# Kernel optimization log

Hardware: AMD Instinct MI355X
Metric: run time of the kernel (lower is better)

## Reference

```python
import jax, jax.numpy as jnp
import numpy as np

N = 4096
HID = 512
NUM_HEADS = 8
HEAD_DIM = HID // NUM_HEADS
SCALING = HID ** (-0.5)


def setup_inputs() -> dict:
    key = jax.random.key(0)
    k0, k1, k2, k3, k4, k5 = jax.random.split(key, 6)
    h = jax.random.normal(k0, (N, HID), dtype=jnp.float32)
    A = (jax.random.uniform(k1, (N, N), dtype=jnp.float32) < 0.01).astype(jnp.float32)
    scale = 0.02
    Wq = jax.random.normal(k2, (HID, HID), dtype=jnp.float32) * scale
    Wk = jax.random.normal(k3, (HID, HID), dtype=jnp.float32) * scale
    Wv = jax.random.normal(k4, (HID, HID), dtype=jnp.float32) * scale
    Wo = jax.random.normal(k5, (HID, HID), dtype=jnp.float32) * scale
    return {"A": A, "h": h, "Wq": Wq, "Wk": Wk, "Wv": Wv, "Wo": Wo}


def reference(A, h, Wq, Wk, Wv, Wo):
    n = h.shape[0]
    # nn.Linear: y = x @ W.T ; reshape(N, head_dim, num_heads) puts heads LAST
    q = (h @ Wq.T).reshape(n, HEAD_DIM, NUM_HEADS) * SCALING  # [N, D, H]
    k = (h @ Wk.T).reshape(n, HEAD_DIM, NUM_HEADS)            # [N, D, H]
    v = (h @ Wv.T).reshape(n, HEAD_DIM, NUM_HEADS)            # [N, D, H]
    # scores = bmm(q^T[H,N,D], k^T[H,D,N]) -> [H, N, N]
    scores = jnp.einsum('ndh,mdh->hnm', q, k)
    # mask by dense multiply (zeros still contribute exp(0) to softmax, as in source)
    attn = jax.nn.softmax(A[None, :, :] * scores, axis=-1)    # [H, N, N]
    # out = bmm(attn, v^T[H,N,D]) -> [H, N, D] -> transpose to [N, D, H]
    out = jnp.einsum('hnm,mdh->ndh', attn, v)                 # [N, D, H]
    out = out.reshape(n, HEAD_DIM * NUM_HEADS) @ Wo.T         # [N, HID]
    return out
```

## Files before the change

### kernel.cpp

```cpp
#include <hip/hip_runtime.h>
#include <hip/hip_bf16.h>


#define N_TOK 4096
#define HID   512
#define NHEAD 8
#define HDIM  64
#define SCALING_F 0.044194173824159216f

#define QH_OFF    0u
#define KVB_OFF   2097152u
#define VSP_OFF   3145728u
#define VSUM_OFF  3162112u
#define CNT_OFF   3162624u
#define LIST_OFF  3166720u
#define HB_OFF    3691008u
#define WQKV_OFF  4739584u
#define WO_OFF    5132800u

typedef __attribute__((ext_vector_type(8))) short bf16x8;
typedef __attribute__((ext_vector_type(4))) float f32x4;
typedef __attribute__((ext_vector_type(2))) float f32x2;

__device__ __forceinline__ ushort f2bf(float f) {
    union { float f; unsigned u; } x; x.f = f;
    const unsigned r = x.u + 0x7fffu + ((x.u >> 16) & 1u);
    return (ushort)(r >> 16);
}

#define GLOAD_LDS16(g, l) \
    __builtin_amdgcn_global_load_lds((const __attribute__((address_space(1))) void*)(g), \
                                     (__attribute__((address_space(3))) void*)(l), 16, 0, 0)

__global__ __launch_bounds__(256) void prep(const float* __restrict__ A,
                                            const float* __restrict__ h,
                                            const float* __restrict__ wq,
                                            const float* __restrict__ wk,
                                            const float* __restrict__ wv,
                                            const float* __restrict__ wo,
                                            float* __restrict__ ws)
{
    const int bx = blockIdx.x;
    if (bx < 1024) {
        int* cnts  = (int*)(ws + CNT_OFF);
        int* lists = (int*)(ws + LIST_OFF);
        const int row  = bx * 4 + (threadIdx.x >> 6);
        const int lane = threadIdx.x & 63;
        const float4* Arow = (const float4*)(A + (size_t)row * N_TOK);
        int* out = lists + (size_t)row * 128;
        int cnt = 0;
#pragma unroll 4
        for (int it = 0; it < 16; ++it) {
            const float4 v = Arow[it * 64 + lane];
            const float vals[4] = {v.x, v.y, v.z, v.w};
#pragma unroll
            for (int j = 0; j < 4; ++j) {
                const bool nz = (vals[j] != 0.0f);
                const unsigned long long mask = __ballot(nz);
                if (nz) {
                    const int pos = cnt + __popcll(mask & ((1ull << lane) - 1ull));
                    if (pos < 128) out[pos] = it * 256 + lane * 4 + j;
                }
                cnt += __popcll(mask);
            }
        }
        if (lane == 0) cnts[row] = (cnt < 128) ? cnt : 128;
        return;
    }

    const int cb    = bx - 1024;
    const int chunk = cb >> 8;
    const int inner = (cb & 255) * 1024 + threadIdx.x * 4;
    ushort* hb    = (ushort*)(ws + HB_OFF);
    ushort* wqkvb = (ushort*)(ws + WQKV_OFF);
    ushort* wob   = (ushort*)(ws + WO_OFF);

    if (chunk < 11) {
        const float* src;
        ushort* dst;
        if (chunk < 8)       { src = h + (size_t)chunk * 262144; dst = hb + (size_t)chunk * 262144; }
        else if (chunk == 8) { src = wq; dst = wqkvb; }
        else if (chunk == 9) { src = wk; dst = wqkvb + 262144; }
        else                 { src = wv; dst = wqkvb + 524288; }
        const float4 v = *(const float4*)&src[inner];
        ushort4 o;
        o.x = f2bf(v.x); o.y = f2bf(v.y); o.z = f2bf(v.z); o.w = f2bf(v.w);
        *(ushort4*)&dst[inner] = o;
    } else {
        const float4 v = *(const float4*)&wo[inner];
        const int o = inner >> 9;
        const int j0 = inner & 511;
        const float vals[4] = {v.x, v.y, v.z, v.w};
#pragma unroll
        for (int jj = 0; jj < 4; ++jj) {
            const int j = j0 + jj;
            wob[o * 512 + (j & 7) * 64 + (j >> 3)] = f2bf(vals[jj]);
        }
    }
}

__global__ __launch_bounds__(256) void qkv_gemm_mfma(const float* __restrict__ ws_ro,
                                                     float* __restrict__ ws)
{
    const ushort* Xb = (const ushort*)(ws_ro + HB_OFF);
    const int z = blockIdx.z;
    const int hh = blockIdx.x;
    const ushort* W = (const ushort*)(ws_ro + WQKV_OFF) + (size_t)z * 262144;

    const int mb = blockIdx.y * 128;

    __shared__ ushort As[128 * 32];
    __shared__ ushort Bs[64 * 32];

    const int t    = threadIdx.x;
    const int w    = t >> 6;
    const int lane = t & 63;
    const int wr   = w >> 1, wc = w & 1;
    const int fr   = lane & 15;
    const int fq   = lane >> 4;
    const int fk   = fq * 8;

    const int srow = w * 16 + (lane >> 2);
    const int scol = (lane & 3) * 8;
    const ushort* gA = Xb + (size_t)(mb + srow) * HID + scol;
    const ushort* gB = W + (size_t)(hh + srow * 8) * HID + scol;
    ushort* lAbase = &As[w * 512];
    ushort* lBbase = &Bs[w * 512];

    f32x4 acc[4][2] = {};

    for (int kb = 0; kb < HID; kb += 32) {
        __syncthreads();
        GLOAD_LDS16(gA + kb,            lAbase);
        GLOAD_LDS16(gA + kb + 64 * HID, lAbase + 2048);
        GLOAD_LDS16(gB + kb,            lBbase);
        __syncthreads();

        bf16x8 a[4], b[2];
#pragma unroll
        for (int mi = 0; mi < 4; ++mi)
            a[mi] = *(const bf16x8*)&As[(wr * 64 + mi * 16 + fr) * 32 + fk];
#pragma unroll
        for (int ni = 0; ni < 2; ++ni)
            b[ni] = *(const bf16x8*)&Bs[(wc * 32 + ni * 16 + fr) * 32 + fk];
#pragma unroll
        for (int mi = 0; mi < 4; ++mi)
#pragma unroll
            for (int ni = 0; ni < 2; ++ni)
                acc[mi][ni] = __builtin_amdgcn_mfma_f32_16x16x32_bf16(a[mi], b[ni], acc[mi][ni], 0, 0, 0);
    }

    if (z == 0) {
        float* Yh = ws + QH_OFF + (size_t)hh * (N_TOK * HDIM);
#pragma unroll
        for (int ni = 0; ni < 2; ++ni) {
            const int d = wc * 32 + ni * 16 + fr;
#pragma unroll
            for (int mi = 0; mi < 4; ++mi) {
                const int r0 = mb + wr * 64 + mi * 16 + fq * 4;
#pragma unroll
                for (int j = 0; j < 4; ++j)
                    Yh[(size_t)(r0 + j) * HDIM + d] = acc[mi][ni][j] * SCALING_F;
            }
        }
    } else {
        unsigned char* KVh = (unsigned char*)(ws + KVB_OFF)
                           + (size_t)hh * (N_TOK * 128) + ((z == 1) ? 0 : 64);
#pragma unroll
        for (int ni = 0; ni < 2; ++ni) {
            const int d = wc * 32 + ni * 16 + fr;
#pragma unroll
            for (int mi = 0; mi < 4; ++mi) {
                const int r0 = mb + wr * 64 + mi * 16 + fq * 4;
#pragma unroll
                for (int j = 0; j < 4; ++j) {
                    const float v = acc[mi][ni][j];
                    const int p = __builtin_amdgcn_cvt_pk_fp8_f32(v, v, 0, false);
                    KVh[(size_t)(r0 + j) * 128 + d] = (unsigned char)(p & 0xff);
                }
            }
        }
        if (z == 2) {
            __syncthreads();
            float* red = (float*)As;
#pragma unroll
            for (int ni = 0; ni < 2; ++ni) {
                float ps = 0.f;
#pragma unroll
                for (int mi = 0; mi < 4; ++mi)
#pragma unroll
                    for (int j = 0; j < 4; ++j) ps += acc[mi][ni][j];
                red[(wr * 4 + fq) * 64 + wc * 32 + ni * 16 + fr] = ps;
            }
            __syncthreads();
            if (t < 64) {
                float s = 0.f;
#pragma unroll
                for (int r = 0; r < 8; ++r) s += red[r * 64 + t];
                ws[VSP_OFF + blockIdx.y * 512 + hh * 64 + t] = s;
            }
        }
    }
}

__global__ __launch_bounds__(64) void vsum_collapse(float* __restrict__ ws)
{
    const float* VSP = ws + VSP_OFF;
    const int hh = blockIdx.x, d = threadIdx.x;
    float s = 0.f;
#pragma unroll
    for (int mb = 0; mb < 32; ++mb) s += VSP[mb * 512 + hh * 64 + d];
    ws[VSUM_OFF + hh * 64 + d] = s;
}

__global__ __launch_bounds__(256) void attn_sparse(float* __restrict__ ws)
{
    const int b    = blockIdx.x;
    const int n    = (b >> 3) * 4 + (b & 3);
    const int hg   = (b >> 2) & 1;
    const int t    = threadIdx.x;
    const int w    = t >> 6;
    const int lane = t & 63;
    const int g    = lane >> 3;
    const int dg   = lane & 7;
    const int h    = hg * 4 + w;

    const int* cnts  = (const int*)(ws + CNT_OFF);
    const int* lists = (const int*)(ws + LIST_OFF);

    __shared__ int s_idx[128];
    const int cnt = cnts[n];
    if (t < 128) s_idx[t] = (t < cnt) ? lists[(size_t)n * 128 + t] : 0;
    __syncthreads();

    const float* Qh = ws + QH_OFF;
    const unsigned char* KVB = (const unsigned char*)(ws + KVB_OFF);
    const unsigned char* kvh = KVB + (size_t)h * (N_TOK * 128);
    ushort* opb = (ushort*)(ws + HB_OFF);

    const float* qrow = Qh + ((size_t)h * N_TOK + n) * HDIM + dg * 8;
    const float4 qa = *(const float4*)qrow;
    const float4 qb = *(const float4*)(qrow + 4);

    float acc[8] = {0.f, 0.f, 0.f, 0.f, 0.f, 0.f, 0.f, 0.f};
    float den = 0.f;

    const int iters = (cnt + 7) >> 3;
    for (int i = 0; i < iters; ++i) {
        const int j = i * 8 + g;
        const int m = s_idx[j < 128 ? j : 127];
        const bool valid = (j < cnt);
        const unsigned char* row = kvh + (size_t)m * 128;
        const uint2 kw = *(const uint2*)(row + dg * 8);
        const uint2 vw = *(const uint2*)(row + 64 + dg * 8);

        const f32x2 k0 = __builtin_amdgcn_cvt_pk_f32_fp8(kw.x, false);
        const f32x2 k1 = __builtin_amdgcn_cvt_pk_f32_fp8(kw.x, true);
        const f32x2 k2 = __builtin_amdgcn_cvt_pk_f32_fp8(kw.y, false);
        const f32x2 k3 = __builtin_amdgcn_cvt_pk_f32_fp8(kw.y, true);
        float s = qa.x * k0[0] + qa.y * k0[1] + qa.z * k1[0] + qa.w * k1[1]
                + qb.x * k2[0] + qb.y * k2[1] + qb.z * k3[0] + qb.w * k3[1];
        s += __shfl_xor(s, 1);
        s += __shfl_xor(s, 2);
        s += __shfl_xor(s, 4);
        const float wgt = valid ? __expf(s) - 1.0f : 0.0f;

        const f32x2 v0 = __builtin_amdgcn_cvt_pk_f32_fp8(vw.x, false);
        const f32x2 v1 = __builtin_amdgcn_cvt_pk_f32_fp8(vw.x, true);
        const f32x2 v2 = __builtin_amdgcn_cvt_pk_f32_fp8(vw.y, false);
        const f32x2 v3 = __builtin_amdgcn_cvt_pk_f32_fp8(vw.y, true);
        acc[0] += wgt * v0[0]; acc[1] += wgt * v0[1];
        acc[2] += wgt * v1[0]; acc[3] += wgt * v1[1];
        acc[4] += wgt * v2[0]; acc[5] += wgt * v2[1];
        acc[6] += wgt * v3[0]; acc[7] += wgt * v3[1];
        den += wgt;
    }

#pragma unroll
    for (int off = 8; off <= 32; off <<= 1) {
#pragma unroll
        for (int e = 0; e < 8; ++e) acc[e] += __shfl_xor(acc[e], off);
        den += __shfl_xor(den, off);
    }

    if (g == 0) {
        const float* vsp = ws + VSUM_OFF + h * 64 + dg * 8;
        const float4 va = *(const float4*)vsp;
        const float4 vb = *(const float4*)(vsp + 4);
        const float vs[8] = {va.x, va.y, va.z, va.w, vb.x, vb.y, vb.z, vb.w};
        const float r = 1.0f / (4096.0f + den);
        bf16x8 o;
#pragma unroll
        for (int e = 0; e < 8; ++e) o[e] = (short)f2bf((vs[e] + acc[e]) * r);
        *(bf16x8*)(opb + (size_t)n * HID + h * 64 + dg * 8) = o;
    }
}

__global__ __launch_bounds__(256) void out_gemm_mfma(const float* __restrict__ ws_ro,
                                                     float* __restrict__ out)
{
    const ushort* Xb = (const ushort*)(ws_ro + HB_OFF);
    const ushort* W  = (const ushort*)(ws_ro + WO_OFF);

    const int nb = blockIdx.x * 64;
    const int mb = blockIdx.y * 128;

    __shared__ ushort As[128 * 32];
    __shared__ ushort Bs[64 * 32];

    const int t    = threadIdx.x;
    const int w    = t >> 6;
    const int lane = t & 63;
    const int wr   = w >> 1, wc = w & 1;
    const int fr   = lane & 15;
    const int fq   = lane >> 4;
    const int fk   = fq * 8;

    const int srow = w * 16 + (lane >> 2);
    const int scol = (lane & 3) * 8;
    const ushort* gA = Xb + (size_t)(mb + srow) * HID + scol;
    const ushort* gB = W  + (size_t)(nb + srow) * HID + scol;
    ushort* lAbase = &As[w * 512];
    ushort* lBbase = &Bs[w * 512];

    f32x4 acc[4][2] = {};

    for (int kb = 0; kb < HID; kb += 32) {
        __syncthreads();
        GLOAD_LDS16(gA + kb,            lAbase);
        GLOAD_LDS16(gA + kb + 64 * HID, lAbase + 2048);
        GLOAD_LDS16(gB + kb,            lBbase);
        __syncthreads();

        bf16x8 a[4], b[2];
#pragma unroll
        for (int mi = 0; mi < 4; ++mi)
            a[mi] = *(const bf16x8*)&As[(wr * 64 + mi * 16 + fr) * 32 + fk];
#pragma unroll
        for (int ni = 0; ni < 2; ++ni)
            b[ni] = *(const bf16x8*)&Bs[(wc * 32 + ni * 16 + fr) * 32 + fk];
#pragma unroll
        for (int mi = 0; mi < 4; ++mi)
#pragma unroll
            for (int ni = 0; ni < 2; ++ni)
                acc[mi][ni] = __builtin_amdgcn_mfma_f32_16x16x32_bf16(a[mi], b[ni], acc[mi][ni], 0, 0, 0);
    }

#pragma unroll
    for (int ni = 0; ni < 2; ++ni) {
        const int col = nb + wc * 32 + ni * 16 + fr;
#pragma unroll
        for (int mi = 0; mi < 4; ++mi) {
            const int r0 = mb + wr * 64 + mi * 16 + fq * 4;
#pragma unroll
            for (int j = 0; j < 4; ++j)
                out[(size_t)(r0 + j) * HID + col] = acc[mi][ni][j];
        }
    }
}

extern "C" void kernel_launch(void* const* d_in, const int* in_sizes, int n_in,
                              void* d_out, int out_size, void* d_ws, size_t ws_size,
                              hipStream_t stream)
{
    const float* A  = (const float*)d_in[0];
    const float* h  = (const float*)d_in[1];
    const float* Wq = (const float*)d_in[2];
    const float* Wk = (const float*)d_in[3];
    const float* Wv = (const float*)d_in[4];
    const float* Wo = (const float*)d_in[5];
    float* out = (float*)d_out;
    float* ws  = (float*)d_ws;

    prep<<<dim3(4096), 256, 0, stream>>>(A, h, Wq, Wk, Wv, Wo, ws);
    qkv_gemm_mfma<<<dim3(8, 32, 3), 256, 0, stream>>>(ws, ws);
    vsum_collapse<<<dim3(8), 64, 0, stream>>>(ws);
    attn_sparse<<<dim3(8192), 256, 0, stream>>>(ws);
    out_gemm_mfma<<<dim3(8, 32), 256, 0, stream>>>(ws, out);
}
```

Measured before the change: 73.18 us.

## Double-buffer GEMM LDS tiles, interleave K/V bytes, unroll sparse attention loop

Both MFMA GEMMs (QKV and output projection) now double-buffer their LDS tiles. The next K-slice's global-to-LDS load is issued before computing on the current slice, which removes one barrier per iteration. The fp8 K/V rows are re-laid out so that each lane's 8 K bytes and 8 V bytes sit next to each other, letting the attention kernel fetch both with a single 16-byte load. The attention loop also processes two neighbors per iteration to raise memory-level parallelism. The cost is twice the LDS per block, which may lower occupancy, plus slightly more register pressure.

```diff
diff --git a/kernel.cpp b/kernel.cpp
--- a/kernel.cpp
+++ b/kernel.cpp
@@ -109,8 +109,7 @@
 
     const int mb = blockIdx.y * 128;
 
-    __shared__ ushort As[128 * 32];
-    __shared__ ushort Bs[64 * 32];
+    __shared__ ushort SM[12288];
 
     const int t    = threadIdx.x;
     const int w    = t >> 6;
@@ -124,31 +123,37 @@
     const int scol = (lane & 3) * 8;
     const ushort* gA = Xb + (size_t)(mb + srow) * HID + scol;
     const ushort* gB = W + (size_t)(hh + srow * 8) * HID + scol;
-    ushort* lAbase = &As[w * 512];
-    ushort* lBbase = &Bs[w * 512];
+
+#define QKV_STAGE(p, kb) do { \
+        ushort* base_ = &SM[(p) * 6144]; \
+        GLOAD_LDS16(gA + (kb),            base_ + w * 512); \
+        GLOAD_LDS16(gA + (kb) + 64 * HID, base_ + 2048 + w * 512); \
+        GLOAD_LDS16(gB + (kb),            base_ + 4096 + w * 512); \
+    } while (0)
 
     f32x4 acc[4][2] = {};
 
-    for (int kb = 0; kb < HID; kb += 32) {
-        __syncthreads();
-        GLOAD_LDS16(gA + kb,            lAbase);
-        GLOAD_LDS16(gA + kb + 64 * HID, lAbase + 2048);
-        GLOAD_LDS16(gB + kb,            lBbase);
-        __syncthreads();
-
+    QKV_STAGE(0, 0);
+    __syncthreads();
+    for (int ts = 0; ts < 16; ++ts) {
+        const int p = ts & 1;
+        if (ts < 15) QKV_STAGE(p ^ 1, (ts + 1) * 32);
+        const ushort* base = &SM[p * 6144];
         bf16x8 a[4], b[2];
 #pragma unroll
         for (int mi = 0; mi < 4; ++mi)
-            a[mi] = *(const bf16x8*)&As[(wr * 64 + mi * 16 + fr) * 32 + fk];
+            a[mi] = *(const bf16x8*)&base[(wr * 64 + mi * 16 + fr) * 32 + fk];
 #pragma unroll
         for (int ni = 0; ni < 2; ++ni)
-            b[ni] = *(const bf16x8*)&Bs[(wc * 32 + ni * 16 + fr) * 32 + fk];
+            b[ni] = *(const bf16x8*)&base[4096 + (wc * 32 + ni * 16 + fr) * 32 + fk];
 #pragma unroll
         for (int mi = 0; mi < 4; ++mi)
 #pragma unroll
             for (int ni = 0; ni < 2; ++ni)
                 acc[mi][ni] = __builtin_amdgcn_mfma_f32_16x16x32_bf16(a[mi], b[ni], acc[mi][ni], 0, 0, 0);
-    }
+        __syncthreads();
+    }
+#undef QKV_STAGE
 
     if (z == 0) {
         float* Yh = ws + QH_OFF + (size_t)hh * (N_TOK * HDIM);
@@ -165,10 +170,11 @@
         }
     } else {
         unsigned char* KVh = (unsigned char*)(ws + KVB_OFF)
-                           + (size_t)hh * (N_TOK * 128) + ((z == 1) ? 0 : 64);
+                           + (size_t)hh * (N_TOK * 128) + ((z == 1) ? 0 : 8);
 #pragma unroll
         for (int ni = 0; ni < 2; ++ni) {
             const int d = wc * 32 + ni * 16 + fr;
+            const int doff = (d >> 3) * 16 + (d & 7);
 #pragma unroll
             for (int mi = 0; mi < 4; ++mi) {
                 const int r0 = mb + wr * 64 + mi * 16 + fq * 4;
@@ -176,13 +182,12 @@
                 for (int j = 0; j < 4; ++j) {
                     const float v = acc[mi][ni][j];
                     const int p = __builtin_amdgcn_cvt_pk_fp8_f32(v, v, 0, false);
-                    KVh[(size_t)(r0 + j) * 128 + d] = (unsigned char)(p & 0xff);
+                    KVh[(size_t)(r0 + j) * 128 + doff] = (unsigned char)(p & 0xff);
                 }
             }
         }
         if (z == 2) {
-            __syncthreads();
-            float* red = (float*)As;
+            float* red = (float*)SM;
 #pragma unroll
             for (int ni = 0; ni < 2; ++ni) {
                 float ps = 0.f;
@@ -234,8 +239,8 @@
     __syncthreads();
 
     const float* Qh = ws + QH_OFF;
-    const unsigned char* KVB = (const unsigned char*)(ws + KVB_OFF);
-    const unsigned char* kvh = KVB + (size_t)h * (N_TOK * 128);
+    const unsigned char* kvh = (const unsigned char*)(ws + KVB_OFF)
+                             + (size_t)h * (N_TOK * 128) + dg * 16;
     ushort* opb = (ushort*)(ws + HB_OFF);
 
     const float* qrow = Qh + ((size_t)h * N_TOK + n) * HDIM + dg * 8;
@@ -246,35 +251,60 @@
     float den = 0.f;
 
     const int iters = (cnt + 7) >> 3;
-    for (int i = 0; i < iters; ++i) {
-        const int j = i * 8 + g;
-        const int m = s_idx[j < 128 ? j : 127];
-        const bool valid = (j < cnt);
-        const unsigned char* row = kvh + (size_t)m * 128;
-        const uint2 kw = *(const uint2*)(row + dg * 8);
-        const uint2 vw = *(const uint2*)(row + 64 + dg * 8);
-
-        const f32x2 k0 = __builtin_amdgcn_cvt_pk_f32_fp8(kw.x, false);
-        const f32x2 k1 = __builtin_amdgcn_cvt_pk_f32_fp8(kw.x, true);
-        const f32x2 k2 = __builtin_amdgcn_cvt_pk_f32_fp8(kw.y, false);
-        const f32x2 k3 = __builtin_amdgcn_cvt_pk_f32_fp8(kw.y, true);
-        float s = qa.x * k0[0] + qa.y * k0[1] + qa.z * k1[0] + qa.w * k1[1]
-                + qb.x * k2[0] + qb.y * k2[1] + qb.z * k3[0] + qb.w * k3[1];
-        s += __shfl_xor(s, 1);
-        s += __shfl_xor(s, 2);
-        s += __shfl_xor(s, 4);
-        const float wgt = valid ? __expf(s) - 1.0f : 0.0f;
-
-        const f32x2 v0 = __builtin_amdgcn_cvt_pk_f32_fp8(vw.x, false);
-        const f32x2 v1 = __builtin_amdgcn_cvt_pk_f32_fp8(vw.x, true);
-        const f32x2 v2 = __builtin_amdgcn_cvt_pk_f32_fp8(vw.y, false);
-        const f32x2 v3 = __builtin_amdgcn_cvt_pk_f32_fp8(vw.y, true);
-        acc[0] += wgt * v0[0]; acc[1] += wgt * v0[1];
-        acc[2] += wgt * v1[0]; acc[3] += wgt * v1[1];
-        acc[4] += wgt * v2[0]; acc[5] += wgt * v2[1];
-        acc[6] += wgt * v3[0]; acc[7] += wgt * v3[1];
-        den += wgt;
-    }
+
+#define ATTN_DOT(kw0, kw1, sval) do { \
+        const f32x2 k0_ = __builtin_amdgcn_cvt_pk_f32_fp8((kw0), false); \
+        const f32x2 k1_ = __builtin_amdgcn_cvt_pk_f32_fp8((kw0), true);  \
+        const f32x2 k2_ = __builtin_amdgcn_cvt_pk_f32_fp8((kw1), false); \
+        const f32x2 k3_ = __builtin_amdgcn_cvt_pk_f32_fp8((kw1), true);  \
+        sval = qa.x * k0_[0] + qa.y * k0_[1] + qa.z * k1_[0] + qa.w * k1_[1] \
+             + qb.x * k2_[0] + qb.y * k2_[1] + qb.z * k3_[0] + qb.w * k3_[1]; \
+        sval += __shfl_xor(sval, 1); \
+        sval += __shfl_xor(sval, 2); \
+        sval += __shfl_xor(sval, 4); \
+    } while (0)
+
+#define ATTN_ACC(vw0, vw1, wgt) do { \
+        const f32x2 v0_ = __builtin_amdgcn_cvt_pk_f32_fp8((vw0), false); \
+        const f32x2 v1_ = __builtin_amdgcn_cvt_pk_f32_fp8((vw0), true);  \
+        const f32x2 v2_ = __builtin_amdgcn_cvt_pk_f32_fp8((vw1), false); \
+        const f32x2 v3_ = __builtin_amdgcn_cvt_pk_f32_fp8((vw1), true);  \
+        acc[0] += (wgt) * v0_[0]; acc[1] += (wgt) * v0_[1]; \
+        acc[2] += (wgt) * v1_[0]; acc[3] += (wgt) * v1_[1]; \
+        acc[4] += (wgt) * v2_[0]; acc[5] += (wgt) * v2_[1]; \
+        acc[6] += (wgt) * v3_[0]; acc[7] += (wgt) * v3_[1]; \
+    } while (0)
+
+    int i = 0;
+    for (; i + 2 <= iters; i += 2) {
+        const int j0 = i * 8 + g;
+        const int j1 = j0 + 8;
+        const int m0 = s_idx[j0];
+        const int m1 = s_idx[j1];
+        const uint4 kv0 = *(const uint4*)(kvh + (size_t)m0 * 128);
+        const uint4 kv1 = *(const uint4*)(kvh + (size_t)m1 * 128);
+        float s0, s1;
+        ATTN_DOT(kv0.x, kv0.y, s0);
+        ATTN_DOT(kv1.x, kv1.y, s1);
+        const float w0 = (j0 < cnt) ? __expf(s0) - 1.0f : 0.0f;
+        const float w1 = (j1 < cnt) ? __expf(s1) - 1.0f : 0.0f;
+        ATTN_ACC(kv0.z, kv0.w, w0);
+        ATTN_ACC(kv1.z, kv1.w, w1);
+        den += w0;
+        den += w1;
+    }
+    if (i < iters) {
+        const int j0 = i * 8 + g;
+        const int m0 = s_idx[j0 & 127];
+        const uint4 kv0 = *(const uint4*)(kvh + (size_t)m0 * 128);
+        float s0;
+        ATTN_DOT(kv0.x, kv0.y, s0);
+        const float w0 = (j0 < cnt) ? __expf(s0) - 1.0f : 0.0f;
+        ATTN_ACC(kv0.z, kv0.w, w0);
+        den += w0;
+    }
+#undef ATTN_DOT
+#undef ATTN_ACC
 
 #pragma unroll
     for (int off = 8; off <= 32; off <<= 1) {
@@ -305,8 +335,7 @@
     const int nb = blockIdx.x * 64;
     const int mb = blockIdx.y * 128;
 
-    __shared__ ushort As[128 * 32];
-    __shared__ ushort Bs[64 * 32];
+    __shared__ ushort SM[12288];
 
     const int t    = threadIdx.x;
     const int w    = t >> 6;
@@ -320,31 +349,37 @@
     const int scol = (lane & 3) * 8;
     const ushort* gA = Xb + (size_t)(mb + srow) * HID + scol;
     const ushort* gB = W  + (size_t)(nb + srow) * HID + scol;
-    ushort* lAbase = &As[w * 512];
-    ushort* lBbase = &Bs[w * 512];
+
+#define OUT_STAGE(p, kb) do { \
+        ushort* base_ = &SM[(p) * 6144]; \
+        GLOAD_LDS16(gA + (kb),            base_ + w * 512); \
+        GLOAD_LDS16(gA + (kb) + 64 * HID, base_ + 2048 + w * 512); \
+        GLOAD_LDS16(gB + (kb),            base_ + 4096 + w * 512); \
+    } while (0)
 
     f32x4 acc[4][2] = {};
 
-    for (int kb = 0; kb < HID; kb += 32) {
-        __syncthreads();
-        GLOAD_LDS16(gA + kb,            lAbase);
-        GLOAD_LDS16(gA + kb + 64 * HID, lAbase + 2048);
-        GLOAD_LDS16(gB + kb,            lBbase);
-        __syncthreads();
-
+    OUT_STAGE(0, 0);
+    __syncthreads();
+    for (int ts = 0; ts < 16; ++ts) {
+        const int p = ts & 1;
+        if (ts < 15) OUT_STAGE(p ^ 1, (ts + 1) * 32);
+        const ushort* base = &SM[p * 6144];
         bf16x8 a[4], b[2];
 #pragma unroll
         for (int mi = 0; mi < 4; ++mi)
-            a[mi] = *(const bf16x8*)&As[(wr * 64 + mi * 16 + fr) * 32 + fk];
+            a[mi] = *(const bf16x8*)&base[(wr * 64 + mi * 16 + fr) * 32 + fk];
 #pragma unroll
         for (int ni = 0; ni < 2; ++ni)
-            b[ni] = *(const bf16x8*)&Bs[(wc * 32 + ni * 16 + fr) * 32 + fk];
+            b[ni] = *(const bf16x8*)&base[4096 + (wc * 32 + ni * 16 + fr) * 32 + fk];
 #pragma unroll
         for (int mi = 0; mi < 4; ++mi)
 #pragma unroll
             for (int ni = 0; ni < 2; ++ni)
                 acc[mi][ni] = __builtin_amdgcn_mfma_f32_16x16x32_bf16(a[mi], b[ni], acc[mi][ni], 0, 0, 0);
-    }
+        __syncthreads();
+    }
+#undef OUT_STAGE
 
 #pragma unroll
     for (int ni = 0; ni < 2; ++ni) {
```

Measured after the change: 68.51 us. 1.07x faster.
